# Performance work log

Hardware: AMD Instinct MI355X
Metric: run time of the kernel (lower is better)

## Reference

```python
import jax, jax.numpy as jnp
import numpy as np

NUM_LABELS = 10  # number of distinct label values in the minibatch
EPS = 1e-8


def setup_inputs() -> dict:
    key = jax.random.key(0)
    k1, k2 = jax.random.split(key)
    z = jax.random.normal(k1, (8192, 20, 256), dtype=jnp.float32)  # [B, C, H]
    labels = jax.random.randint(k2, (8192,), 0, NUM_LABELS)  # [B]
    return {"z": z, "labels": labels}


def reference(z, labels):
    # CODI minibatch loss, positive pairs, representation space.
    # Equivalent to: for each unique label, mse(z[group] + 1e-8, mean(z[group]))
    # summed over labels. Vectorized as a single segment-mean +
    # gather-broadcast + segment-SSE pass (one traversal of z).
    z = jnp.nan_to_num(z)
    B, C, H = z.shape
    counts = jax.ops.segment_sum(
        jnp.ones((B,), dtype=z.dtype), labels, num_segments=NUM_LABELS
    )  # [K]
    sums = jax.ops.segment_sum(z, labels, num_segments=NUM_LABELS)  # [K, C, H]
    means = jnp.nan_to_num(sums / jnp.maximum(counts, 1.0)[:, None, None])
    # per-sample squared distance to its group's mean (note the +EPS as in torch)
    d = (z + EPS) - means[labels]  # [B, C, H]
    per_sample = jnp.sum(d * d, axis=(1, 2))  # [B]
    sse = jax.ops.segment_sum(per_sample, labels, num_segments=NUM_LABELS)  # [K]
    # nn.MSELoss is a mean over all elements of the group: count_k * C * H
    mse_k = sse / (jnp.maximum(counts, 1.0) * (C * H))
    # torch.unique only visits labels present in the batch -> mask empty groups
    return jnp.sum(jnp.where(counts > 0, jnp.nan_to_num(mse_k), 0.0))
```

## Files before the change

kernel.cpp:

```cpp
#include <hip/hip_runtime.h>

#define B_SZ   8192
#define CH     5120
#define CH4    1280
#define K_LAB  10
#define EPS    1e-8f
#define FLTMAX 3.402823466e38f

#define NTHR   320
#define PS     64
#define ST     2


__global__ __launch_bounds__(640) void codi_setup(
    const int* __restrict__ labels, int* __restrict__ idx,
    int* __restrict__ off, float* __restrict__ SSQ, float* __restrict__ nsq,
    int* __restrict__ done)
{
    __shared__ int lab_s[B_SZ];
    __shared__ int cnts[K_LAB];
    __shared__ int offs[K_LAB + 1];
    const int tid  = threadIdx.x;
    const int k    = tid >> 6;
    const int lane = tid & 63;

    const int4* l4 = (const int4*)labels;
    for (int i = tid; i < B_SZ / 4; i += 640) ((int4*)lab_s)[i] = l4[i];
    __syncthreads();

    int cnt = 0;
    for (int b0 = 0; b0 < B_SZ; b0 += 64)
        cnt += __popcll(__ballot(lab_s[b0 + lane] == k));
    if (lane == 0) cnts[k] = cnt;
    __syncthreads();
    if (tid == 0) {
        int a = 0;
        for (int j = 0; j < K_LAB; ++j) { offs[j] = a; a += cnts[j]; }
        offs[K_LAB] = a;
    }
    __syncthreads();

    int base = offs[k];
    const unsigned long long ltmask = (1ULL << lane) - 1ULL;
    for (int b0 = 0; b0 < B_SZ; b0 += 64) {
        int lab = lab_s[b0 + lane];
        unsigned long long m = __ballot(lab == k);
        if (lab == k) idx[base + __popcll(m & ltmask)] = b0 + lane;
        base += __popcll(m);
    }
    if (tid < K_LAB + 1) off[tid] = offs[tid];
    if (tid < K_LAB) { SSQ[tid] = 0.f; nsq[tid] = 0.f; }
    if (tid == 0) *done = 0;
}

__global__ __launch_bounds__(NTHR) void codi_gather(
    const float4* __restrict__ z4, const int* __restrict__ idx,
    const int* __restrict__ off, float4* __restrict__ S_part,
    float* __restrict__ SSQ)
{
    const int tid = threadIdx.x;
    const int k   = blockIdx.x / PS;
    const int ps  = blockIdx.x % PS;

    const int kb  = off[k];
    const int cnt = off[k + 1] - kb;
    const int s0  = kb + (int)(((long long)cnt * ps) / PS);
    const int s1  = kb + (int)(((long long)cnt * (ps + 1)) / PS);
    const int n   = s1 - s0;

    __shared__ int rows[160];
    for (int i = tid; i < n; i += NTHR) rows[i] = idx[s0 + i];
    __syncthreads();

    float4 sum[4];
    #pragma unroll
    for (int j = 0; j < 4; ++j) sum[j] = make_float4(0.f, 0.f, 0.f, 0.f);
    float ssq = 0.f;

#define ISSUE(BUF, W, S_) do { \
        _Pragma("unroll") \
        for (int u = 0; u < ST; ++u) { \
            int i_ = (S_) * ST + u; \
            int ic_ = (i_ < n) ? i_ : n - 1; \
            W[u] = (i_ < n) ? 1.f : 0.f; \
            const size_t rb_ = (size_t)rows[ic_] * CH4; \
            _Pragma("unroll") \
            for (int j = 0; j < 4; ++j) BUF[u][j] = z4[rb_ + j * NTHR + tid]; \
        } } while (0)

#define CONSUME(BUF, W) do { \
        _Pragma("unroll") \
        for (int u = 0; u < ST; ++u) { \
            _Pragma("unroll") \
            for (int j = 0; j < 4; ++j) { \
                float4 v = BUF[u][j]; \
                v.x = (v.x == v.x) ? fminf(fmaxf(v.x, -FLTMAX), FLTMAX) : 0.f; \
                v.y = (v.y == v.y) ? fminf(fmaxf(v.y, -FLTMAX), FLTMAX) : 0.f; \
                v.z = (v.z == v.z) ? fminf(fmaxf(v.z, -FLTMAX), FLTMAX) : 0.f; \
                v.w = (v.w == v.w) ? fminf(fmaxf(v.w, -FLTMAX), FLTMAX) : 0.f; \
                v.x *= W[u]; v.y *= W[u]; v.z *= W[u]; v.w *= W[u]; \
                sum[j].x += v.x; sum[j].y += v.y; \
                sum[j].z += v.z; sum[j].w += v.w; \
                ssq = fmaf(v.x, v.x, ssq); ssq = fmaf(v.y, v.y, ssq); \
                ssq = fmaf(v.z, v.z, ssq); ssq = fmaf(v.w, v.w, ssq); \
            } \
        } } while (0)

    if (n > 0) {
        const int nst = (n + ST - 1) / ST;
        float4 A[ST][4], B[ST][4];
        float  wa[ST], wb[ST];
        ISSUE(A, wa, 0);
        int s = 0;
        while (s + 1 < nst) {
            ISSUE(B, wb, s + 1);
            CONSUME(A, wa);
            if (s + 2 < nst) ISSUE(A, wa, s + 2);
            CONSUME(B, wb);
            s += 2;
        }
        if (s < nst) CONSUME(A, wa);
    }
#undef ISSUE
#undef CONSUME

    float4* sp = S_part + (size_t)blockIdx.x * CH4;
    #pragma unroll
    for (int j = 0; j < 4; ++j) sp[j * NTHR + tid] = sum[j];

    #pragma unroll
    for (int o = 32; o > 0; o >>= 1) ssq += __shfl_down(ssq, o, 64);
    if ((tid & 63) == 0) atomicAdd(&SSQ[k], ssq);
}

__global__ __launch_bounds__(NTHR) void codi_reduce(
    const float4* __restrict__ S_part, float* __restrict__ nsq,
    const float* __restrict__ SSQ, const int* __restrict__ off,
    int* __restrict__ done, float* __restrict__ out)
{
    const int tid = threadIdx.x;
    const int k   = blockIdx.x >> 2;
    const int cc  = blockIdx.x & 3;
    __shared__ float wsum[5];

    float4 s = make_float4(0.f, 0.f, 0.f, 0.f);
    #pragma unroll 8
    for (int ps = 0; ps < PS; ++ps) {
        float4 v = S_part[((size_t)(k * PS + ps)) * CH4 + cc * NTHR + tid];
        s.x += v.x; s.y += v.y; s.z += v.z; s.w += v.w;
    }
    float w = fmaf(s.x, s.x, fmaf(s.y, s.y, fmaf(s.z, s.z, s.w * s.w)));
    #pragma unroll
    for (int o = 32; o > 0; o >>= 1) w += __shfl_down(w, o, 64);
    if ((tid & 63) == 0) wsum[tid >> 6] = w;
    __syncthreads();

    if (tid == 0) {
        atomicAdd(&nsq[k], wsum[0] + wsum[1] + wsum[2] + wsum[3] + wsum[4]);
        __threadfence();
        int t = atomicAdd(done, 1);
        if (t == K_LAB * 4 - 1) {
            float loss = 0.f;
            for (int kk = 0; kk < K_LAB; ++kk) {
                float nn = (float)(off[kk + 1] - off[kk]);
                if (nn > 0.f) {
                    float ns  = atomicAdd(&nsq[kk], 0.f);
                    float sse = SSQ[kk] - ns / nn + nn * (float)CH * (EPS * EPS);
                    float mse = sse / (nn * (float)CH);
                    if (mse == mse) loss += mse;
                }
            }
            out[0] = loss;
        }
    }
}

extern "C" void kernel_launch(void* const* d_in, const int* in_sizes, int n_in,
                              void* d_out, int out_size, void* d_ws, size_t ws_size,
                              hipStream_t stream) {
    const float4* z4     = (const float4*)d_in[0];
    const int*    labels = (const int*)d_in[1];

    float* hdr    = (float*)d_ws;
    float* SSQ    = hdr;
    float* nsq    = hdr + 16;
    int*   off    = (int*)(hdr + 32);
    int*   done   = (int*)(hdr + 48);
    int*   idx    = (int*)(hdr + 64);
    float* S_part = hdr + 64 + B_SZ;

    codi_setup<<<1, 640, 0, stream>>>(labels, idx, off, SSQ, nsq, done);
    codi_gather<<<K_LAB * PS, NTHR, 0, stream>>>(
        z4, idx, off, (float4*)S_part, SSQ);
    codi_reduce<<<K_LAB * 4, NTHR, 0, stream>>>(
        (const float4*)S_part, nsq, SSQ, off, done, (float*)d_out);
}
```

Baseline: 269.9 us.

## Replace label-sorted gather with streaming per-chunk segmented accumulation over all labels

Drops the single-block setup kernel that builds a label-sorted index. The main pass now streams contiguous 64-row chunks of z and keeps per-label accumulators in registers for all ten labels, selected by a wave-uniform label. Partial sums, squared sums and counts are written per chunk, and a second kernel reduces them and finalises the loss with a ticket counter. This removes the serial setup launch and the scattered row gathers, at the cost of ten accumulators per thread (higher register pressure) and a larger partial-sum buffer to reduce.

```diff
diff --git a/kernel.cpp b/kernel.cpp
--- a/kernel.cpp
+++ b/kernel.cpp
@@ -7,171 +7,163 @@
 #define EPS    1e-8f
 #define FLTMAX 3.402823466e38f
 
-#define NTHR   320
-#define PS     64
-#define ST     2
+#define RC_N   128
+#define ROWS   64
+#define CC_N   4
+#define CCW    320
+#define NT1    320
+
+#define CG_N   20
+#define NT2    64
+#define RCSTRIDE (K_LAB * CC_N * CCW)
 
 
-__global__ __launch_bounds__(640) void codi_setup(
-    const int* __restrict__ labels, int* __restrict__ idx,
-    int* __restrict__ off, float* __restrict__ SSQ, float* __restrict__ nsq,
-    int* __restrict__ done)
+__device__ __forceinline__ float4 sanitize(float4 v) {
+    v.x = (v.x == v.x) ? fminf(fmaxf(v.x, -FLTMAX), FLTMAX) : 0.f;
+    v.y = (v.y == v.y) ? fminf(fmaxf(v.y, -FLTMAX), FLTMAX) : 0.f;
+    v.z = (v.z == v.z) ? fminf(fmaxf(v.z, -FLTMAX), FLTMAX) : 0.f;
+    v.w = (v.w == v.w) ? fminf(fmaxf(v.w, -FLTMAX), FLTMAX) : 0.f;
+    return v;
+}
+
+__global__ __launch_bounds__(NT1) void codi_pass1(
+    const float4* __restrict__ z4, const int* __restrict__ labels,
+    float4* __restrict__ P_sum, float* __restrict__ P_ssq,
+    int* __restrict__ P_cnt, int* __restrict__ done)
 {
-    __shared__ int lab_s[B_SZ];
-    __shared__ int cnts[K_LAB];
-    __shared__ int offs[K_LAB + 1];
-    const int tid  = threadIdx.x;
-    const int k    = tid >> 6;
-    const int lane = tid & 63;
+    const int tid = threadIdx.x;
+    const int rc  = blockIdx.x >> 2;
+    const int cc  = blockIdx.x & 3;
 
-    const int4* l4 = (const int4*)labels;
-    for (int i = tid; i < B_SZ / 4; i += 640) ((int4*)lab_s)[i] = l4[i];
+    __shared__ int   lab_s[ROWS];
+    __shared__ float wssq[5][K_LAB];
+
+    if (blockIdx.x == 0 && tid == 0) *done = 0;
+
+    if (tid < ROWS) lab_s[tid] = labels[rc * ROWS + tid];
     __syncthreads();
 
-    int cnt = 0;
-    for (int b0 = 0; b0 < B_SZ; b0 += 64)
-        cnt += __popcll(__ballot(lab_s[b0 + lane] == k));
-    if (lane == 0) cnts[k] = cnt;
-    __syncthreads();
-    if (tid == 0) {
-        int a = 0;
-        for (int j = 0; j < K_LAB; ++j) { offs[j] = a; a += cnts[j]; }
-        offs[K_LAB] = a;
+    float4 sum[K_LAB];
+    float  ssq[K_LAB];
+    #pragma unroll
+    for (int k = 0; k < K_LAB; ++k) {
+        sum[k] = make_float4(0.f, 0.f, 0.f, 0.f);
+        ssq[k] = 0.f;
+    }
+
+    const float4* zp = z4 + (size_t)rc * ROWS * CH4 + cc * CCW + tid;
+
+    for (int r = 0; r < ROWS; r += 8) {
+        float4 v[8];
+        #pragma unroll
+        for (int u = 0; u < 8; ++u) v[u] = zp[(size_t)(r + u) * CH4];
+
+        #pragma unroll
+        for (int u = 0; u < 8; ++u) {
+            const int lab = __builtin_amdgcn_readfirstlane(lab_s[r + u]);
+            float4 t = sanitize(v[u]);
+            float  q = fmaf(t.x, t.x, fmaf(t.y, t.y, fmaf(t.z, t.z, t.w * t.w)));
+            #pragma unroll
+            for (int k = 0; k < K_LAB; ++k) {
+                const float w = (lab == k) ? 1.f : 0.f;
+                sum[k].x = fmaf(t.x, w, sum[k].x);
+                sum[k].y = fmaf(t.y, w, sum[k].y);
+                sum[k].z = fmaf(t.z, w, sum[k].z);
+                sum[k].w = fmaf(t.w, w, sum[k].w);
+                ssq[k]   = fmaf(q,   w, ssq[k]);
+            }
+        }
+    }
+
+    #pragma unroll
+    for (int k = 0; k < K_LAB; ++k)
+        P_sum[(((size_t)rc * K_LAB + k) * CC_N + cc) * CCW + tid] = sum[k];
+
+    const int lane = tid & 63, wid = tid >> 6;
+    #pragma unroll
+    for (int k = 0; k < K_LAB; ++k) {
+        float s = ssq[k];
+        #pragma unroll
+        for (int o = 32; o > 0; o >>= 1) s += __shfl_down(s, o, 64);
+        if (lane == 0) wssq[wid][k] = s;
     }
     __syncthreads();
+    if (tid < K_LAB) {
+        float s = wssq[0][tid] + wssq[1][tid] + wssq[2][tid]
+                + wssq[3][tid] + wssq[4][tid];
+        P_ssq[(rc * CC_N + cc) * K_LAB + tid] = s;
+    }
 
-    int base = offs[k];
-    const unsigned long long ltmask = (1ULL << lane) - 1ULL;
-    for (int b0 = 0; b0 < B_SZ; b0 += 64) {
-        int lab = lab_s[b0 + lane];
-        unsigned long long m = __ballot(lab == k);
-        if (lab == k) idx[base + __popcll(m & ltmask)] = b0 + lane;
-        base += __popcll(m);
+    if (cc == 0 && tid < 64) {
+        const int lab = lab_s[tid];
+        #pragma unroll
+        for (int k = 0; k < K_LAB; ++k) {
+            unsigned long long m = __ballot(lab == k);
+            if (tid == k) P_cnt[rc * K_LAB + k] = __popcll(m);
+        }
     }
-    if (tid < K_LAB + 1) off[tid] = offs[tid];
-    if (tid < K_LAB) { SSQ[tid] = 0.f; nsq[tid] = 0.f; }
-    if (tid == 0) *done = 0;
 }
 
-__global__ __launch_bounds__(NTHR) void codi_gather(
-    const float4* __restrict__ z4, const int* __restrict__ idx,
-    const int* __restrict__ off, float4* __restrict__ S_part,
-    float* __restrict__ SSQ)
-{
-    const int tid = threadIdx.x;
-    const int k   = blockIdx.x / PS;
-    const int ps  = blockIdx.x % PS;
-
-    const int kb  = off[k];
-    const int cnt = off[k + 1] - kb;
-    const int s0  = kb + (int)(((long long)cnt * ps) / PS);
-    const int s1  = kb + (int)(((long long)cnt * (ps + 1)) / PS);
-    const int n   = s1 - s0;
-
-    __shared__ int rows[160];
-    for (int i = tid; i < n; i += NTHR) rows[i] = idx[s0 + i];
-    __syncthreads();
-
-    float4 sum[4];
-    #pragma unroll
-    for (int j = 0; j < 4; ++j) sum[j] = make_float4(0.f, 0.f, 0.f, 0.f);
-    float ssq = 0.f;
-
-#define ISSUE(BUF, W, S_) do { \
-        _Pragma("unroll") \
-        for (int u = 0; u < ST; ++u) { \
-            int i_ = (S_) * ST + u; \
-            int ic_ = (i_ < n) ? i_ : n - 1; \
-            W[u] = (i_ < n) ? 1.f : 0.f; \
-            const size_t rb_ = (size_t)rows[ic_] * CH4; \
-            _Pragma("unroll") \
-            for (int j = 0; j < 4; ++j) BUF[u][j] = z4[rb_ + j * NTHR + tid]; \
-        } } while (0)
-
-#define CONSUME(BUF, W) do { \
-        _Pragma("unroll") \
-        for (int u = 0; u < ST; ++u) { \
-            _Pragma("unroll") \
-            for (int j = 0; j < 4; ++j) { \
-                float4 v = BUF[u][j]; \
-                v.x = (v.x == v.x) ? fminf(fmaxf(v.x, -FLTMAX), FLTMAX) : 0.f; \
-                v.y = (v.y == v.y) ? fminf(fmaxf(v.y, -FLTMAX), FLTMAX) : 0.f; \
-                v.z = (v.z == v.z) ? fminf(fmaxf(v.z, -FLTMAX), FLTMAX) : 0.f; \
-                v.w = (v.w == v.w) ? fminf(fmaxf(v.w, -FLTMAX), FLTMAX) : 0.f; \
-                v.x *= W[u]; v.y *= W[u]; v.z *= W[u]; v.w *= W[u]; \
-                sum[j].x += v.x; sum[j].y += v.y; \
-                sum[j].z += v.z; sum[j].w += v.w; \
-                ssq = fmaf(v.x, v.x, ssq); ssq = fmaf(v.y, v.y, ssq); \
-                ssq = fmaf(v.z, v.z, ssq); ssq = fmaf(v.w, v.w, ssq); \
-            } \
-        } } while (0)
-
-    if (n > 0) {
-        const int nst = (n + ST - 1) / ST;
-        float4 A[ST][4], B[ST][4];
-        float  wa[ST], wb[ST];
-        ISSUE(A, wa, 0);
-        int s = 0;
-        while (s + 1 < nst) {
-            ISSUE(B, wb, s + 1);
-            CONSUME(A, wa);
-            if (s + 2 < nst) ISSUE(A, wa, s + 2);
-            CONSUME(B, wb);
-            s += 2;
-        }
-        if (s < nst) CONSUME(A, wa);
-    }
-#undef ISSUE
-#undef CONSUME
-
-    float4* sp = S_part + (size_t)blockIdx.x * CH4;
-    #pragma unroll
-    for (int j = 0; j < 4; ++j) sp[j * NTHR + tid] = sum[j];
-
-    #pragma unroll
-    for (int o = 32; o > 0; o >>= 1) ssq += __shfl_down(ssq, o, 64);
-    if ((tid & 63) == 0) atomicAdd(&SSQ[k], ssq);
-}
-
-__global__ __launch_bounds__(NTHR) void codi_reduce(
-    const float4* __restrict__ S_part, float* __restrict__ nsq,
-    const float* __restrict__ SSQ, const int* __restrict__ off,
+__global__ __launch_bounds__(NT2) void codi_pass2(
+    const float4* __restrict__ P_sum, const float* __restrict__ P_ssq,
+    const int* __restrict__ P_cnt, float* __restrict__ pn,
+    float* __restrict__ ssqk, float* __restrict__ cntk,
     int* __restrict__ done, float* __restrict__ out)
 {
     const int tid = threadIdx.x;
-    const int k   = blockIdx.x >> 2;
-    const int cc  = blockIdx.x & 3;
-    __shared__ float wsum[5];
+    const int k   = blockIdx.x / CG_N;
+    const int cg  = blockIdx.x % CG_N;
+    const int c   = cg * NT2 + tid;
+    const int cc  = c / CCW;
+    const int co  = c % CCW;
 
+    const float4* p = P_sum + ((size_t)k * CC_N + cc) * CCW + co;
     float4 s = make_float4(0.f, 0.f, 0.f, 0.f);
-    #pragma unroll 8
-    for (int ps = 0; ps < PS; ++ps) {
-        float4 v = S_part[((size_t)(k * PS + ps)) * CH4 + cc * NTHR + tid];
+    #pragma unroll 16
+    for (int rc = 0; rc < RC_N; ++rc) {
+        float4 v = p[(size_t)rc * RCSTRIDE];
         s.x += v.x; s.y += v.y; s.z += v.z; s.w += v.w;
     }
-    float w = fmaf(s.x, s.x, fmaf(s.y, s.y, fmaf(s.z, s.z, s.w * s.w)));
+    float q = fmaf(s.x, s.x, fmaf(s.y, s.y, fmaf(s.z, s.z, s.w * s.w)));
     #pragma unroll
-    for (int o = 32; o > 0; o >>= 1) w += __shfl_down(w, o, 64);
-    if ((tid & 63) == 0) wsum[tid >> 6] = w;
+    for (int o = 32; o > 0; o >>= 1) q += __shfl_down(q, o, 64);
+    if (tid == 0) pn[k * CG_N + cg] = q;
+
+    if (cg == 0) {
+        float s2 = 0.f;
+        for (int i = tid; i < RC_N * CC_N; i += NT2) s2 += P_ssq[i * K_LAB + k];
+        #pragma unroll
+        for (int o = 32; o > 0; o >>= 1) s2 += __shfl_down(s2, o, 64);
+        int n = 0;
+        for (int i = tid; i < RC_N; i += NT2) n += P_cnt[i * K_LAB + k];
+        #pragma unroll
+        for (int o = 32; o > 0; o >>= 1) n += __shfl_down(n, o, 64);
+        if (tid == 0) { ssqk[k] = s2; cntk[k] = (float)n; }
+    }
+
+    __threadfence();
+    __shared__ int ticket;
+    if (tid == 0) ticket = atomicAdd(done, 1);
     __syncthreads();
 
-    if (tid == 0) {
-        atomicAdd(&nsq[k], wsum[0] + wsum[1] + wsum[2] + wsum[3] + wsum[4]);
-        __threadfence();
-        int t = atomicAdd(done, 1);
-        if (t == K_LAB * 4 - 1) {
-            float loss = 0.f;
-            for (int kk = 0; kk < K_LAB; ++kk) {
-                float nn = (float)(off[kk + 1] - off[kk]);
+    if (ticket == K_LAB * CG_N - 1) {
+        float acc = 0.f;
+        for (int k2 = 0; k2 < K_LAB; ++k2) {
+            float np = 0.f;
+            if (tid < CG_N) np = atomicAdd(&pn[k2 * CG_N + tid], 0.f);
+            #pragma unroll
+            for (int o = 32; o > 0; o >>= 1) np += __shfl_down(np, o, 64);
+            if (tid == 0) {
+                float nn = atomicAdd(&cntk[k2], 0.f);
+                float s2 = atomicAdd(&ssqk[k2], 0.f);
                 if (nn > 0.f) {
-                    float ns  = atomicAdd(&nsq[kk], 0.f);
-                    float sse = SSQ[kk] - ns / nn + nn * (float)CH * (EPS * EPS);
+                    float sse = s2 - np / nn + nn * (float)CH * (EPS * EPS);
                     float mse = sse / (nn * (float)CH);
-                    if (mse == mse) loss += mse;
+                    if (mse == mse) acc += mse;
                 }
             }
-            out[0] = loss;
         }
+        if (tid == 0) out[0] = acc;
     }
 }
 
@@ -181,17 +173,16 @@
     const float4* z4     = (const float4*)d_in[0];
     const int*    labels = (const int*)d_in[1];
 
-    float* hdr    = (float*)d_ws;
-    float* SSQ    = hdr;
-    float* nsq    = hdr + 16;
-    int*   off    = (int*)(hdr + 32);
-    int*   done   = (int*)(hdr + 48);
-    int*   idx    = (int*)(hdr + 64);
-    float* S_part = hdr + 64 + B_SZ;
+    float*  hdr   = (float*)d_ws;
+    int*    done  = (int*)hdr;
+    float*  pn    = hdr + 16;
+    float*  ssqk  = hdr + 224;
+    float*  cntk  = hdr + 240;
+    int*    P_cnt = (int*)(hdr + 256);
+    float*  P_ssq = hdr + 1536;
+    float4* P_sum = (float4*)(hdr + 6720);
 
-    codi_setup<<<1, 640, 0, stream>>>(labels, idx, off, SSQ, nsq, done);
-    codi_gather<<<K_LAB * PS, NTHR, 0, stream>>>(
-        z4, idx, off, (float4*)S_part, SSQ);
-    codi_reduce<<<K_LAB * 4, NTHR, 0, stream>>>(
-        (const float4*)S_part, nsq, SSQ, off, done, (float*)d_out);
+    codi_pass1<<<RC_N * CC_N, NT1, 0, stream>>>(z4, labels, P_sum, P_ssq, P_cnt, done);
+    codi_pass2<<<K_LAB * CG_N, NT2, 0, stream>>>(P_sum, P_ssq, P_cnt, pn, ssqk,
+                                                 cntk, done, (float*)d_out);
 }
```

Result: no change. 272.6 us (+1.0%).
